# Performance work log

Hardware: AMD Instinct MI355X
Metric: run time of the kernel (lower is better)

## Reference

```python
import jax, jax.numpy as jnp
import numpy as np

N_NODES = 100000


def _gcn_layer(x, W, b, src, dst, n):
    # symmetric normalization (add_self_loops=False): deg = in-degree at dst
    deg = jax.ops.segment_sum(jnp.ones_like(src, dtype=x.dtype), dst, num_segments=n)
    dis = jnp.where(deg > 0, jax.lax.rsqrt(jnp.maximum(deg, 1.0)), 0.0)
    h = x @ W                                    # [N, out]
    norm = dis[src] * dis[dst]                   # [E]
    msg = h[src] * norm[:, None]                 # [E, out]
    out = jax.ops.segment_sum(msg, dst, num_segments=n)
    return out + b


def setup_inputs() -> dict:
    key = jax.random.key(0)
    k1, k2, k3, k4, k5, k6 = jax.random.split(key, 6)
    F_IN, HID, OUT = 64, 64, 2
    x = jax.random.normal(k1, (N_NODES, F_IN), dtype=jnp.float32)
    edge_index = jax.random.randint(k2, (2, 1600000), 0, N_NODES, dtype=jnp.int64)
    s1 = 1.0 / np.sqrt(2 * F_IN)
    s2 = 1.0 / np.sqrt(HID)
    W1 = jax.random.uniform(k3, (2 * F_IN, HID), jnp.float32, -s1, s1)
    b1 = jax.random.uniform(k4, (HID,), jnp.float32, -s1, s1)
    W2 = jax.random.uniform(k5, (HID, OUT), jnp.float32, -s2, s2)
    b2 = jax.random.uniform(k6, (OUT,), jnp.float32, -s2, s2)
    return {"x": x, "edge_index": edge_index, "W1": W1, "b1": b1, "W2": W2, "b2": b2}


def reference(x, edge_index, W1, b1, W2, b2):
    n = x.shape[0]
    src, dst = edge_index[0], edge_index[1]
    # global mean pool broadcast to every node, concat on feature dim -> [N, 2F]
    mean = jnp.mean(x, axis=0, keepdims=True)
    complete = jnp.concatenate([x, jnp.broadcast_to(mean, x.shape)], axis=1)
    h = _gcn_layer(complete, W1, b1, src, dst, n)
    h = jax.nn.relu(h)
    out = _gcn_layer(h, W2, b2, src, dst, n)
    return out
```

## Files before the change

### kernel.cpp

```cpp
#include <hip/hip_runtime.h>


#define BKT        128
#define BKT_SHIFT  10
#define NPB        1024
#define BKT_CAP    18432
#define CHUNK      4096
#define EPT        8
#define CS_BLK     64
#define CUR_STRIDE 32

__device__ __forceinline__ unsigned short f2bf(float v) {
    unsigned u = __float_as_uint(v);
    u += 0x7FFFu + ((u >> 16) & 1u);
    return (unsigned short)(u >> 16);
}
__device__ __forceinline__ float bf2f(unsigned short h) {
    return __uint_as_float((unsigned)h << 16);
}

__global__ __launch_bounds__(512) void bucketAC_kernel(
        const int* __restrict__ src, const int* __restrict__ dst,
        int e, unsigned* __restrict__ pairs, int* __restrict__ cursor,
        const float* __restrict__ x, float* __restrict__ sums, int n) {
    int tid = threadIdx.x;
    if (blockIdx.x < CS_BLK) {
        __shared__ float4 s4[512];
        int cb = blockIdx.x;
        const float4* x4 = (const float4*)x;
        int total4 = n * 16;
        float4 acc = make_float4(0.f, 0.f, 0.f, 0.f);
        for (int i = cb * 512 + tid; i < total4; i += CS_BLK * 512) {
            float4 v = x4[i];
            acc.x += v.x; acc.y += v.y; acc.z += v.z; acc.w += v.w;
        }
        s4[tid] = acc;
        __syncthreads();
        if (tid < 16) {
            float4 v = s4[tid];
            for (int k = 1; k < 32; ++k) {
                float4 w = s4[tid + 16 * k];
                v.x += w.x; v.y += w.y; v.z += w.z; v.w += w.w;
            }
            atomicAdd(&sums[tid * 4 + 0], v.x);
            atomicAdd(&sums[tid * 4 + 1], v.y);
            atomicAdd(&sums[tid * 4 + 2], v.z);
            atomicAdd(&sums[tid * 4 + 3], v.w);
        }
        return;
    }
    __shared__ int cnt[BKT], sb[BKT], gpos[BKT];
    __shared__ unsigned stage[CHUNK];
    __shared__ unsigned char bb[CHUNK];
    int chunkStart = (blockIdx.x - CS_BLK) * CHUNK;
    int v = e - chunkStart;
    if (v > CHUNK) v = CHUNK;
    if (tid < BKT) cnt[tid] = 0;
    __syncthreads();
    int myb[EPT], myoff[EPT];
    unsigned myp[EPT];
#pragma unroll
    for (int t = 0; t < EPT; ++t) {
        int i = chunkStart + t * 512 + tid;
        myb[t] = -1;
        if (i < e) {
            int s = src[i], d = dst[i];
            myb[t] = d >> BKT_SHIFT;
            myp[t] = ((unsigned)s << BKT_SHIFT) | (unsigned)(d & (NPB - 1));
            myoff[t] = atomicAdd(&cnt[myb[t]], 1);
        }
    }
    __syncthreads();
    if (tid < BKT) sb[tid] = cnt[tid];
    __syncthreads();
    for (int off = 1; off < BKT; off <<= 1) {
        int t = (tid < BKT && tid >= off) ? sb[tid - off] : 0;
        __syncthreads();
        if (tid < BKT) sb[tid] += t;
        __syncthreads();
    }
    if (tid < BKT) {
        int excl = tid ? sb[tid - 1] : 0;
        int gb = atomicAdd(&cursor[tid * CUR_STRIDE], cnt[tid]);
        gpos[tid] = tid * BKT_CAP + gb - excl;
        cnt[tid] = excl;
    }
    __syncthreads();
#pragma unroll
    for (int t = 0; t < EPT; ++t) {
        if (myb[t] >= 0) {
            int p = cnt[myb[t]] + myoff[t];
            stage[p] = myp[t];
            bb[p] = (unsigned char)myb[t];
        }
    }
    __syncthreads();
    for (int j = tid; j < v; j += 512) {
        pairs[gpos[bb[j]] + j] = stage[j];
    }
}

__global__ __launch_bounds__(512) void csrB_kernel(
        const unsigned* __restrict__ pairs, const int* __restrict__ cursor,
        float* __restrict__ dis, int* __restrict__ rowstart,
        int* __restrict__ eidx, int n,
        const float* __restrict__ sums, const float* __restrict__ W1,
        float* __restrict__ cvec) {
    __shared__ int ldeg[NPB];
    __shared__ int lcur[NPB];
    __shared__ int scanbuf[512];
    __shared__ int s_ebase;
    int b = blockIdx.x;
    int tid = threadIdx.x;
    int node0 = b << BKT_SHIFT;
    if (node0 >= n) return;
    int nl = n - node0;
    if (nl > NPB) nl = NPB;
    int cnt_b = cursor[b * CUR_STRIDE];
    for (int i = tid; i < NPB; i += 512) ldeg[i] = 0;
    if (tid == 0) s_ebase = 0;
    __syncthreads();
    if (tid < b) atomicAdd(&s_ebase, cursor[tid * CUR_STRIDE]);
    const unsigned* mp = pairs + (size_t)b * BKT_CAP;
    for (int i = tid; i < cnt_b; i += 512)
        atomicAdd(&ldeg[mp[i] & (NPB - 1)], 1);
    __syncthreads();
    int base = tid * 2;
    int ts = ldeg[base] + ldeg[base + 1];
    scanbuf[tid] = ts;
    __syncthreads();
    for (int off = 1; off < 512; off <<= 1) {
        int t = (tid >= off) ? scanbuf[tid - off] : 0;
        __syncthreads();
        scanbuf[tid] += t;
        __syncthreads();
    }
    int ex = tid ? scanbuf[tid - 1] : 0;
    int ebase = s_ebase;
#pragma unroll
    for (int j = 0; j < 2; ++j) {
        lcur[base + j] = ex;
        if (base + j < nl) {
            int dv = ldeg[base + j];
            rowstart[node0 + base + j] = ebase + ex;
            dis[node0 + base + j] = dv > 0 ? rsqrtf((float)dv) : 0.f;
        }
        ex += ldeg[base + j];
    }
    if (tid == 0 && node0 + NPB >= n)
        rowstart[n] = ebase + cnt_b;
    __syncthreads();
    for (int i = tid; i < cnt_b; i += 512) {
        unsigned p = mp[i];
        int pos = atomicAdd(&lcur[p & (NPB - 1)], 1);
        eidx[ebase + pos] = (int)(p >> BKT_SHIFT);
    }
    if (b == 0 && tid < 64) {
        float inv_n = 1.0f / (float)n;
        float acc = 0.f;
        for (int k = 0; k < 64; ++k) acc += (sums[k] * inv_n) * W1[(64 + k) * 64 + tid];
        cvec[tid] = acc;
    }
}

__global__ __launch_bounds__(256, 4) void gemm1_kernel(
        const float* __restrict__ x, const float* __restrict__ W1,
        const float* __restrict__ c, const float* __restrict__ dis,
        unsigned short* __restrict__ h1s, int n) {
    __shared__ float Ws[64 * 64];
    __shared__ float Xs[64 * 68];
    int tid = threadIdx.x;
    int row0 = blockIdx.x * 64;
    {
        const float4* w4 = (const float4*)W1;
        float4* s4 = (float4*)Ws;
        for (int i = tid; i < 1024; i += 256) s4[i] = w4[i];
    }
    for (int i = tid; i < 1024; i += 256) {
        int r = i >> 4, c4 = (i & 15) * 4;
        int gr = row0 + r;
        float4 xv = make_float4(0.f, 0.f, 0.f, 0.f);
        if (gr < n) xv = *(const float4*)&x[(size_t)gr * 64 + c4];
        *(float4*)&Xs[r * 68 + c4] = xv;
    }
    __syncthreads();
    int c16 = tid & 15;
    int rb = (tid >> 4) * 4;
    float4 cj = ((const float4*)c)[c16];
    float4 a0 = cj, a1 = cj, a2 = cj, a3 = cj;
#pragma unroll 4
    for (int k = 0; k < 64; ++k) {
        float4 w = *(const float4*)&Ws[k * 64 + c16 * 4];
        float x0 = Xs[(rb + 0) * 68 + k];
        float x1 = Xs[(rb + 1) * 68 + k];
        float x2 = Xs[(rb + 2) * 68 + k];
        float x3 = Xs[(rb + 3) * 68 + k];
        a0.x += x0 * w.x; a0.y += x0 * w.y; a0.z += x0 * w.z; a0.w += x0 * w.w;
        a1.x += x1 * w.x; a1.y += x1 * w.y; a1.z += x1 * w.z; a1.w += x1 * w.w;
        a2.x += x2 * w.x; a2.y += x2 * w.y; a2.z += x2 * w.z; a2.w += x2 * w.w;
        a3.x += x3 * w.x; a3.y += x3 * w.y; a3.z += x3 * w.z; a3.w += x3 * w.w;
    }
    float4 accs[4] = {a0, a1, a2, a3};
#pragma unroll
    for (int r = 0; r < 4; ++r) {
        int gr = row0 + rb + r;
        if (gr < n) {
            float dv = dis[gr];
            float4 o = accs[r];
            ushort4 hs;
            hs.x = f2bf(o.x * dv);
            hs.y = f2bf(o.y * dv);
            hs.z = f2bf(o.z * dv);
            hs.w = f2bf(o.w * dv);
            *(ushort4*)&h1s[(size_t)gr * 64 + c16 * 4] = hs;
        }
    }
}

__global__ void gather1_kernel(const int* __restrict__ rowstart,
                               const int* __restrict__ eidx, const float* __restrict__ dis,
                               const unsigned short* __restrict__ h1s,
                               const float* __restrict__ b1, const float* __restrict__ W2,
                               float* __restrict__ h2s, int n) {
    int lane = threadIdx.x & 63;
    int node = blockIdx.x * 4 + (threadIdx.x >> 6);
    if (node >= n) return;
    int rs = rowstart[node];
    int re = rowstart[node + 1];
    int dn = re - rs;
    int m = dn < 64 ? dn : 64;
    int eHeld = (lane < m) ? eidx[rs + lane] : 0;
    int g  = lane >> 4;
    int fb = (lane & 15) * 4;
    float4 acc = make_float4(0.f, 0.f, 0.f, 0.f);
    int j = 0;
    for (; j + 16 <= m; j += 16) {
        int s0 = __shfl(eHeld, j + g, 64);
        int s1 = __shfl(eHeld, j + 4 + g, 64);
        int s2 = __shfl(eHeld, j + 8 + g, 64);
        int s3 = __shfl(eHeld, j + 12 + g, 64);
        ushort4 h0 = *(const ushort4*)&h1s[((size_t)s0 << 6) + fb];
        ushort4 h1 = *(const ushort4*)&h1s[((size_t)s1 << 6) + fb];
        ushort4 h2 = *(const ushort4*)&h1s[((size_t)s2 << 6) + fb];
        ushort4 h3 = *(const ushort4*)&h1s[((size_t)s3 << 6) + fb];
        acc.x += (bf2f(h0.x) + bf2f(h1.x)) + (bf2f(h2.x) + bf2f(h3.x));
        acc.y += (bf2f(h0.y) + bf2f(h1.y)) + (bf2f(h2.y) + bf2f(h3.y));
        acc.z += (bf2f(h0.z) + bf2f(h1.z)) + (bf2f(h2.z) + bf2f(h3.z));
        acc.w += (bf2f(h0.w) + bf2f(h1.w)) + (bf2f(h2.w) + bf2f(h3.w));
    }
    for (; j + 8 <= m; j += 8) {
        int s0 = __shfl(eHeld, j + g, 64);
        int s1 = __shfl(eHeld, j + 4 + g, 64);
        ushort4 h0 = *(const ushort4*)&h1s[((size_t)s0 << 6) + fb];
        ushort4 h1 = *(const ushort4*)&h1s[((size_t)s1 << 6) + fb];
        acc.x += bf2f(h0.x) + bf2f(h1.x);
        acc.y += bf2f(h0.y) + bf2f(h1.y);
        acc.z += bf2f(h0.z) + bf2f(h1.z);
        acc.w += bf2f(h0.w) + bf2f(h1.w);
    }
    for (; j < m; j += 4) {
        int jj = j + g;
        int s = __shfl(eHeld, jj < m ? jj : 0, 64);
        if (jj < m) {
            ushort4 h = *(const ushort4*)&h1s[((size_t)s << 6) + fb];
            acc.x += bf2f(h.x);
            acc.y += bf2f(h.y);
            acc.z += bf2f(h.z);
            acc.w += bf2f(h.w);
        }
    }
    for (int t = 64; t < dn; ++t) {
        if (g == 0) {
            int s = eidx[rs + t];
            ushort4 h = *(const ushort4*)&h1s[((size_t)s << 6) + fb];
            acc.x += bf2f(h.x);
            acc.y += bf2f(h.y);
            acc.z += bf2f(h.z);
            acc.w += bf2f(h.w);
        }
    }
    acc.x += __shfl_xor(acc.x, 16, 64); acc.x += __shfl_xor(acc.x, 32, 64);
    acc.y += __shfl_xor(acc.y, 16, 64); acc.y += __shfl_xor(acc.y, 32, 64);
    acc.z += __shfl_xor(acc.z, 16, 64); acc.z += __shfl_xor(acc.z, 32, 64);
    acc.w += __shfl_xor(acc.w, 16, 64); acc.w += __shfl_xor(acc.w, 32, 64);
    float di = dis[node];
    float4 bv = ((const float4*)b1)[lane & 15];
    float4 w0 = ((const float4*)W2)[(lane & 15) * 2];
    float4 w1 = ((const float4*)W2)[(lane & 15) * 2 + 1];
    float t0 = fmaxf(di * acc.x + bv.x, 0.f);
    float t1 = fmaxf(di * acc.y + bv.y, 0.f);
    float t2 = fmaxf(di * acc.z + bv.z, 0.f);
    float t3 = fmaxf(di * acc.w + bv.w, 0.f);
    float v0 = t0 * w0.x + t1 * w0.z + t2 * w1.x + t3 * w1.z;
    float v1 = t0 * w0.y + t1 * w0.w + t2 * w1.y + t3 * w1.w;
#pragma unroll
    for (int off = 1; off <= 8; off <<= 1) {
        v0 += __shfl_xor(v0, off, 64);
        v1 += __shfl_xor(v1, off, 64);
    }
    if (lane == 0) {
        h2s[(size_t)node * 2 + 0] = di * v0;
        h2s[(size_t)node * 2 + 1] = di * v1;
    }
}

__global__ void gather2_kernel(const int* __restrict__ rowstart,
                               const int* __restrict__ eidx, const float* __restrict__ dis,
                               const float* __restrict__ h2s, const float* __restrict__ b2,
                               float* __restrict__ out, int n) {
    int i = blockIdx.x * blockDim.x + threadIdx.x;
    if (i >= n) return;
    int rs = rowstart[i];
    int dn = rowstart[i + 1] - rs;
    float a0 = 0.f, a1 = 0.f, b0 = 0.f, b1v = 0.f;
    int j = 0;
    for (; j + 2 <= dn; j += 2) {
        int s0 = eidx[rs + j];
        int s1 = eidx[rs + j + 1];
        a0 += h2s[(size_t)s0 * 2 + 0];
        a1 += h2s[(size_t)s0 * 2 + 1];
        b0 += h2s[(size_t)s1 * 2 + 0];
        b1v += h2s[(size_t)s1 * 2 + 1];
    }
    if (j < dn) {
        int s0 = eidx[rs + j];
        a0 += h2s[(size_t)s0 * 2 + 0];
        a1 += h2s[(size_t)s0 * 2 + 1];
    }
    float di = dis[i];
    out[(size_t)i * 2 + 0] = di * (a0 + b0) + b2[0];
    out[(size_t)i * 2 + 1] = di * (a1 + b1v) + b2[1];
}

extern "C" void kernel_launch(void* const* d_in, const int* in_sizes, int n_in,
                              void* d_out, int out_size, void* d_ws, size_t ws_size,
                              hipStream_t stream) {
    const float* x  = (const float*)d_in[0];
    const int*   ei = (const int*)d_in[1];
    const float* W1 = (const float*)d_in[2];
    const float* b1 = (const float*)d_in[3];
    const float* W2 = (const float*)d_in[4];
    const float* b2 = (const float*)d_in[5];
    float* out = (float*)d_out;

    const int n = in_sizes[0] / 64;
    const int e = in_sizes[1] / 2;
    const int* srcI = ei;
    const int* dstI = ei + e;

    char* p = (char*)d_ws;
    int* rowstart = (int*)p;    p += ((size_t)(n + 1) * 4 + 255) & ~255ull;
    float* dis    = (float*)p;  p += ((size_t)n * 4 + 255) & ~255ull;
    float* sums   = (float*)p;
    int* cursor   = (int*)(p + 256);
    char* zbase   = p;          p += 256 + BKT * CUR_STRIDE * 4;
    float* cvec   = (float*)p;  p += 256;
    int* eidx     = (int*)p;    p += ((size_t)e * 4 + 255) & ~255ull;
    unsigned* pairs      = (unsigned*)p;
    unsigned short* h1s  = (unsigned short*)p;
    {
        size_t pairs_sz = (size_t)BKT * BKT_CAP * 4;
        size_t h1s_sz   = (size_t)n * 64 * 2;
        size_t u = pairs_sz > h1s_sz ? pairs_sz : h1s_sz;
        p += (u + 255) & ~255ull;
    }
    float* h2s    = (float*)p;

    hipMemsetAsync(zbase, 0, 256 + BKT * CUR_STRIDE * 4, stream);

    const int nchunks = (e + CHUNK - 1) / CHUNK;
    const int nbkt    = (n + NPB - 1) / NPB;

    bucketAC_kernel<<<CS_BLK + nchunks, 512, 0, stream>>>(srcI, dstI, e, pairs, cursor,
                                                          x, sums, n);
    csrB_kernel<<<nbkt, 512, 0, stream>>>(pairs, cursor, dis, rowstart, eidx, n,
                                          sums, W1, cvec);
    gemm1_kernel<<<(n + 63) / 64, 256, 0, stream>>>(x, W1, cvec, dis, h1s, n);
    gather1_kernel<<<(n + 3) / 4, 256, 0, stream>>>(rowstart, eidx, dis, h1s, b1, W2, h2s, n);
    gather2_kernel<<<(n + 255) / 256, 256, 0, stream>>>(rowstart, eidx, dis, h2s, b2, out, n);
}
```

Baseline: 200.7 us.

## Use bf16 MFMA for first GEMM and shrink dst buckets to 256 nodes

```diff
diff --git a/kernel.cpp b/kernel.cpp
--- a/kernel.cpp
+++ b/kernel.cpp
@@ -1,15 +1,18 @@
 #include <hip/hip_runtime.h>
 
 
-#define BKT        128
-#define BKT_SHIFT  10
-#define NPB        1024
-#define BKT_CAP    18432
+#define NPB        256
+#define NPB_SHIFT  8
+#define BKTS       512
+#define BKT_CAP    5120
 #define CHUNK      4096
 #define EPT        8
 #define CS_BLK     64
 #define CUR_STRIDE 32
 
+using bf16x8 = __attribute__((ext_vector_type(8))) short;
+using f32x4  = __attribute__((ext_vector_type(4))) float;
+
 __device__ __forceinline__ unsigned short f2bf(float v) {
     unsigned u = __float_as_uint(v);
     u += 0x7FFFu + ((u >> 16) & 1u);
@@ -22,7 +25,8 @@
 __global__ __launch_bounds__(512) void bucketAC_kernel(
         const int* __restrict__ src, const int* __restrict__ dst,
         int e, unsigned* __restrict__ pairs, int* __restrict__ cursor,
-        const float* __restrict__ x, float* __restrict__ sums, int n) {
+        const float* __restrict__ x, float* __restrict__ sums,
+        const float* __restrict__ W1, unsigned short* __restrict__ wtg, int n) {
     int tid = threadIdx.x;
     if (blockIdx.x < CS_BLK) {
         __shared__ float4 s4[512];
@@ -49,13 +53,20 @@
         }
         return;
     }
-    __shared__ int cnt[BKT], sb[BKT], gpos[BKT];
+    if (blockIdx.x == CS_BLK) {
+        for (int i = tid; i < 4096; i += 512) {
+            int k = i >> 6, j = i & 63;
+            wtg[j * 64 + k] = f2bf(W1[k * 64 + j]);
+        }
+        return;
+    }
+    __shared__ int cnt[BKTS], sb[BKTS], gpos[BKTS];
     __shared__ unsigned stage[CHUNK];
-    __shared__ unsigned char bb[CHUNK];
-    int chunkStart = (blockIdx.x - CS_BLK) * CHUNK;
+    __shared__ unsigned short bb[CHUNK];
+    int chunkStart = (blockIdx.x - CS_BLK - 1) * CHUNK;
     int v = e - chunkStart;
     if (v > CHUNK) v = CHUNK;
-    if (tid < BKT) cnt[tid] = 0;
+    cnt[tid] = 0;
     __syncthreads();
     int myb[EPT], myoff[EPT];
     unsigned myp[EPT];
@@ -65,24 +76,27 @@
         myb[t] = -1;
         if (i < e) {
             int s = src[i], d = dst[i];
-            myb[t] = d >> BKT_SHIFT;
-            myp[t] = ((unsigned)s << BKT_SHIFT) | (unsigned)(d & (NPB - 1));
+            myb[t] = d >> NPB_SHIFT;
+            myp[t] = ((unsigned)s << NPB_SHIFT) | (unsigned)(d & (NPB - 1));
             myoff[t] = atomicAdd(&cnt[myb[t]], 1);
         }
     }
     __syncthreads();
-    if (tid < BKT) sb[tid] = cnt[tid];
-    __syncthreads();
-    for (int off = 1; off < BKT; off <<= 1) {
-        int t = (tid < BKT && tid >= off) ? sb[tid - off] : 0;
+    sb[tid] = cnt[tid];
+    __syncthreads();
+    for (int off = 1; off < BKTS; off <<= 1) {
+        int t = (tid >= off) ? sb[tid - off] : 0;
         __syncthreads();
-        if (tid < BKT) sb[tid] += t;
+        sb[tid] += t;
         __syncthreads();
     }
-    if (tid < BKT) {
+    {
         int excl = tid ? sb[tid - 1] : 0;
-        int gb = atomicAdd(&cursor[tid * CUR_STRIDE], cnt[tid]);
-        gpos[tid] = tid * BKT_CAP + gb - excl;
+        int cb = cnt[tid];
+        if (cb > 0) {
+            int gb = atomicAdd(&cursor[tid * CUR_STRIDE], cb);
+            gpos[tid] = tid * BKT_CAP + gb - excl;
+        }
         cnt[tid] = excl;
     }
     __syncthreads();
@@ -91,12 +105,14 @@
         if (myb[t] >= 0) {
             int p = cnt[myb[t]] + myoff[t];
             stage[p] = myp[t];
-            bb[p] = (unsigned char)myb[t];
+            bb[p] = (unsigned short)myb[t];
         }
     }
     __syncthreads();
     for (int j = tid; j < v; j += 512) {
-        pairs[gpos[bb[j]] + j] = stage[j];
+        int bk = bb[j];
+        int wi = gpos[bk] + j;
+        if (wi < (bk + 1) * BKT_CAP) pairs[wi] = stage[j];
     }
 }
 
@@ -112,12 +128,13 @@
     __shared__ int s_ebase;
     int b = blockIdx.x;
     int tid = threadIdx.x;
-    int node0 = b << BKT_SHIFT;
+    int node0 = b << NPB_SHIFT;
     if (node0 >= n) return;
     int nl = n - node0;
     if (nl > NPB) nl = NPB;
     int cnt_b = cursor[b * CUR_STRIDE];
-    for (int i = tid; i < NPB; i += 512) ldeg[i] = 0;
+    if (cnt_b > BKT_CAP) cnt_b = BKT_CAP;
+    if (tid < NPB) ldeg[tid] = 0;
     if (tid == 0) s_ebase = 0;
     __syncthreads();
     if (tid < b) atomicAdd(&s_ebase, cursor[tid * CUR_STRIDE]);
@@ -125,9 +142,7 @@
     for (int i = tid; i < cnt_b; i += 512)
         atomicAdd(&ldeg[mp[i] & (NPB - 1)], 1);
     __syncthreads();
-    int base = tid * 2;
-    int ts = ldeg[base] + ldeg[base + 1];
-    scanbuf[tid] = ts;
+    scanbuf[tid] = (tid < NPB) ? ldeg[tid] : 0;
     __syncthreads();
     for (int off = 1; off < 512; off <<= 1) {
         int t = (tid >= off) ? scanbuf[tid - off] : 0;
@@ -135,17 +150,15 @@
         scanbuf[tid] += t;
         __syncthreads();
     }
-    int ex = tid ? scanbuf[tid - 1] : 0;
     int ebase = s_ebase;
-#pragma unroll
-    for (int j = 0; j < 2; ++j) {
-        lcur[base + j] = ex;
-        if (base + j < nl) {
-            int dv = ldeg[base + j];
-            rowstart[node0 + base + j] = ebase + ex;
-            dis[node0 + base + j] = dv > 0 ? rsqrtf((float)dv) : 0.f;
-        }
-        ex += ldeg[base + j];
+    if (tid < NPB) {
+        int ex = tid ? scanbuf[tid - 1] : 0;
+        lcur[tid] = ex;
+        if (tid < nl) {
+            int dv = ldeg[tid];
+            rowstart[node0 + tid] = ebase + ex;
+            dis[node0 + tid] = dv > 0 ? rsqrtf((float)dv) : 0.f;
+        }
     }
     if (tid == 0 && node0 + NPB >= n)
         rowstart[n] = ebase + cnt_b;
@@ -153,7 +166,7 @@
     for (int i = tid; i < cnt_b; i += 512) {
         unsigned p = mp[i];
         int pos = atomicAdd(&lcur[p & (NPB - 1)], 1);
-        eidx[ebase + pos] = (int)(p >> BKT_SHIFT);
+        eidx[ebase + pos] = (int)(p >> NPB_SHIFT);
     }
     if (b == 0 && tid < 64) {
         float inv_n = 1.0f / (float)n;
@@ -163,56 +176,60 @@
     }
 }
 
-__global__ __launch_bounds__(256, 4) void gemm1_kernel(
-        const float* __restrict__ x, const float* __restrict__ W1,
+__global__ __launch_bounds__(256) void gemm1_kernel(
+        const float* __restrict__ x, const unsigned short* __restrict__ wtg,
         const float* __restrict__ c, const float* __restrict__ dis,
         unsigned short* __restrict__ h1s, int n) {
-    __shared__ float Ws[64 * 64];
-    __shared__ float Xs[64 * 68];
+    __shared__ unsigned short Xs[64 * 72];
+    __shared__ unsigned short Ws[64 * 72];
     int tid = threadIdx.x;
     int row0 = blockIdx.x * 64;
-    {
-        const float4* w4 = (const float4*)W1;
-        float4* s4 = (float4*)Ws;
-        for (int i = tid; i < 1024; i += 256) s4[i] = w4[i];
-    }
     for (int i = tid; i < 1024; i += 256) {
-        int r = i >> 4, c4 = (i & 15) * 4;
+        int j = i >> 4, k4 = (i & 15) * 4;
+        *(ushort4*)&Ws[j * 72 + k4] = *(const ushort4*)&wtg[j * 64 + k4];
+    }
+    for (int i = tid; i < 1024; i += 256) {
+        int r = i >> 4, k4 = (i & 15) * 4;
         int gr = row0 + r;
         float4 xv = make_float4(0.f, 0.f, 0.f, 0.f);
-        if (gr < n) xv = *(const float4*)&x[(size_t)gr * 64 + c4];
-        *(float4*)&Xs[r * 68 + c4] = xv;
-    }
-    __syncthreads();
-    int c16 = tid & 15;
-    int rb = (tid >> 4) * 4;
-    float4 cj = ((const float4*)c)[c16];
-    float4 a0 = cj, a1 = cj, a2 = cj, a3 = cj;
-#pragma unroll 4
-    for (int k = 0; k < 64; ++k) {
-        float4 w = *(const float4*)&Ws[k * 64 + c16 * 4];
-        float x0 = Xs[(rb + 0) * 68 + k];
-        float x1 = Xs[(rb + 1) * 68 + k];
-        float x2 = Xs[(rb + 2) * 68 + k];
-        float x3 = Xs[(rb + 3) * 68 + k];
-        a0.x += x0 * w.x; a0.y += x0 * w.y; a0.z += x0 * w.z; a0.w += x0 * w.w;
-        a1.x += x1 * w.x; a1.y += x1 * w.y; a1.z += x1 * w.z; a1.w += x1 * w.w;
-        a2.x += x2 * w.x; a2.y += x2 * w.y; a2.z += x2 * w.z; a2.w += x2 * w.w;
-        a3.x += x3 * w.x; a3.y += x3 * w.y; a3.z += x3 * w.z; a3.w += x3 * w.w;
-    }
-    float4 accs[4] = {a0, a1, a2, a3};
+        if (gr < n) xv = *(const float4*)&x[(size_t)gr * 64 + k4];
+        ushort4 hv;
+        hv.x = f2bf(xv.x); hv.y = f2bf(xv.y); hv.z = f2bf(xv.z); hv.w = f2bf(xv.w);
+        *(ushort4*)&Xs[r * 72 + k4] = hv;
+    }
+    __syncthreads();
+    int lane = tid & 63;
+    int wv = tid >> 6;
+    int l15 = lane & 15;
+    int quad = lane >> 4;
+    f32x4 acc0 = {0.f, 0.f, 0.f, 0.f}, acc1 = acc0, acc2 = acc0, acc3 = acc0;
+    int xrow = wv * 16 + l15;
 #pragma unroll
-    for (int r = 0; r < 4; ++r) {
-        int gr = row0 + rb + r;
-        if (gr < n) {
-            float dv = dis[gr];
-            float4 o = accs[r];
+    for (int ks = 0; ks < 2; ++ks) {
+        bf16x8 bfrag = *(const bf16x8*)&Xs[xrow * 72 + ks * 32 + quad * 8];
+        bf16x8 a0 = *(const bf16x8*)&Ws[(0 * 16 + l15) * 72 + ks * 32 + quad * 8];
+        bf16x8 a1 = *(const bf16x8*)&Ws[(1 * 16 + l15) * 72 + ks * 32 + quad * 8];
+        bf16x8 a2 = *(const bf16x8*)&Ws[(2 * 16 + l15) * 72 + ks * 32 + quad * 8];
+        bf16x8 a3 = *(const bf16x8*)&Ws[(3 * 16 + l15) * 72 + ks * 32 + quad * 8];
+        acc0 = __builtin_amdgcn_mfma_f32_16x16x32_bf16(a0, bfrag, acc0, 0, 0, 0);
+        acc1 = __builtin_amdgcn_mfma_f32_16x16x32_bf16(a1, bfrag, acc1, 0, 0, 0);
+        acc2 = __builtin_amdgcn_mfma_f32_16x16x32_bf16(a2, bfrag, acc2, 0, 0, 0);
+        acc3 = __builtin_amdgcn_mfma_f32_16x16x32_bf16(a3, bfrag, acc3, 0, 0, 0);
+    }
+    int grow = row0 + xrow;
+    if (grow < n) {
+        float dv = dis[grow];
+        const float4* c4 = (const float4*)c;
+        f32x4 accs[4] = {acc0, acc1, acc2, acc3};
+#pragma unroll
+        for (int t = 0; t < 4; ++t) {
+            float4 cj = c4[t * 4 + quad];
             ushort4 hs;
-            hs.x = f2bf(o.x * dv);
-            hs.y = f2bf(o.y * dv);
-            hs.z = f2bf(o.z * dv);
-            hs.w = f2bf(o.w * dv);
-            *(ushort4*)&h1s[(size_t)gr * 64 + c16 * 4] = hs;
+            hs.x = f2bf((accs[t][0] + cj.x) * dv);
+            hs.y = f2bf((accs[t][1] + cj.y) * dv);
+            hs.z = f2bf((accs[t][2] + cj.z) * dv);
+            hs.w = f2bf((accs[t][3] + cj.w) * dv);
+            *(ushort4*)&h1s[(size_t)grow * 64 + t * 16 + quad * 4] = hs;
         }
     }
 }
@@ -347,35 +364,37 @@
     const int e = in_sizes[1] / 2;
     const int* srcI = ei;
     const int* dstI = ei + e;
+    const int nbkt = (n + NPB - 1) >> NPB_SHIFT;
 
     char* p = (char*)d_ws;
     int* rowstart = (int*)p;    p += ((size_t)(n + 1) * 4 + 255) & ~255ull;
     float* dis    = (float*)p;  p += ((size_t)n * 4 + 255) & ~255ull;
     float* sums   = (float*)p;
     int* cursor   = (int*)(p + 256);
-    char* zbase   = p;          p += 256 + BKT * CUR_STRIDE * 4;
+    size_t zsize  = 256 + (size_t)nbkt * CUR_STRIDE * 4;
+    char* zbase   = p;          p += (zsize + 255) & ~255ull;
     float* cvec   = (float*)p;  p += 256;
+    unsigned short* wtg = (unsigned short*)p;  p += (4096 * 2 + 255) & ~255ull;
     int* eidx     = (int*)p;    p += ((size_t)e * 4 + 255) & ~255ull;
     unsigned* pairs      = (unsigned*)p;
     unsigned short* h1s  = (unsigned short*)p;
     {
-        size_t pairs_sz = (size_t)BKT * BKT_CAP * 4;
+        size_t pairs_sz = (size_t)nbkt * BKT_CAP * 4;
         size_t h1s_sz   = (size_t)n * 64 * 2;
         size_t u = pairs_sz > h1s_sz ? pairs_sz : h1s_sz;
         p += (u + 255) & ~255ull;
     }
     float* h2s    = (float*)p;
 
-    hipMemsetAsync(zbase, 0, 256 + BKT * CUR_STRIDE * 4, stream);
+    hipMemsetAsync(zbase, 0, zsize, stream);
 
     const int nchunks = (e + CHUNK - 1) / CHUNK;
-    const int nbkt    = (n + NPB - 1) / NPB;
-
-    bucketAC_kernel<<<CS_BLK + nchunks, 512, 0, stream>>>(srcI, dstI, e, pairs, cursor,
-                                                          x, sums, n);
+
+    bucketAC_kernel<<<CS_BLK + 1 + nchunks, 512, 0, stream>>>(srcI, dstI, e, pairs, cursor,
+                                                              x, sums, W1, wtg, n);
     csrB_kernel<<<nbkt, 512, 0, stream>>>(pairs, cursor, dis, rowstart, eidx, n,
                                           sums, W1, cvec);
-    gemm1_kernel<<<(n + 63) / 64, 256, 0, stream>>>(x, W1, cvec, dis, h1s, n);
+    gemm1_kernel<<<(n + 63) / 64, 256, 0, stream>>>(x, wtg, cvec, dis, h1s, n);
     gather1_kernel<<<(n + 3) / 4, 256, 0, stream>>>(rowstart, eidx, dis, h1s, b1, W2, h2s, n);
     gather2_kernel<<<(n + 255) / 256, 256, 0, stream>>>(rowstart, eidx, dis, h2s, b2, out, n);
 }
```

After: 187.1 us. 1.07x faster.
